# Kernel optimization log

Hardware: AMD Instinct MI355X
Metric: run time of the kernel (lower is better)

## Reference

```python
import jax, jax.numpy as jnp
import numpy as np

ALPHA = 0.2        # LeakyReLU slope inside attention layers
OUT_SLOPE = 0.01   # F.leaky_relu default slope on the final output
EPS = 1e-16        # guards isolated nodes (pyGAT divides by rowsum directly)


def _sp_layer(x, src, dst, W, a, concat, n_nodes):
    # x: [N, F_in], W: [F_in, F_out], a: [2*F_out]
    h = x @ W                                            # [N, F_out]
    eh = jnp.concatenate([h[src], h[dst]], axis=1)       # [E, 2*F_out]
    e = jnp.exp(-jax.nn.leaky_relu(eh @ a, ALPHA))       # [E] unnormalized attn
    denom = jax.ops.segment_sum(e, src, num_segments=n_nodes)          # [N]
    agg = jax.ops.segment_sum(e[:, None] * h[dst], src, num_segments=n_nodes)  # [N, F_out]
    hp = agg / (denom[:, None] + EPS)
    return jax.nn.elu(hp) if concat else hp


def _forward_one(xb, eib, W_heads, a_heads, W_out, a_out):
    n = xb.shape[0]
    src, dst = eib[0], eib[1]
    # independent heads (static small loop), concat on feature dim
    heads = [_sp_layer(xb, src, dst, W_heads[h], a_heads[h], True, n)
             for h in range(W_heads.shape[0])]
    xc = jnp.concatenate(heads, axis=1)                  # [N, nheads*nhid]
    out = _sp_layer(xc, src, dst, W_out, a_out, False, n)  # [N, nclass]
    return jax.nn.leaky_relu(out, OUT_SLOPE)


def setup_inputs() -> dict:
    key = jax.random.key(0)
    B, N, E = 8, 10000, 160000
    nfeat, nhid, nclass, nheads = 256, 64, 64, 8
    ks = jax.random.split(key, 6)
    x = jax.random.normal(ks[0], (B, N, nfeat), dtype=jnp.float32)
    edge_index = jax.random.randint(ks[1], (B, 2, E), 0, N, dtype=jnp.int32)
    # xavier-normal-ish init scales
    W_heads = jax.random.normal(ks[2], (nheads, nfeat, nhid), dtype=jnp.float32) * np.sqrt(2.0 / (nfeat + nhid))
    a_heads = jax.random.normal(ks[3], (nheads, 2 * nhid), dtype=jnp.float32) * np.sqrt(2.0 / (2 * nhid + 1))
    W_out = jax.random.normal(ks[4], (nheads * nhid, nclass), dtype=jnp.float32) * np.sqrt(2.0 / (nheads * nhid + nclass))
    a_out = jax.random.normal(ks[5], (2 * nclass,), dtype=jnp.float32) * np.sqrt(2.0 / (2 * nclass + 1))
    return {"x": x, "edge_index": edge_index, "W_heads": W_heads,
            "a_heads": a_heads, "W_out": W_out, "a_out": a_out, "batch_size": B}


def reference(x, edge_index, W_heads, a_heads, W_out, a_out, batch_size):
    # batch loop in the original is a pure map over graphs -> vmap
    return jax.vmap(lambda xb, eib: _forward_one(xb, eib, W_heads, a_heads, W_out, a_out))(x, edge_index)
```

## Files before the change

kernel.cpp:

```cpp
#include <hip/hip_runtime.h>
#include <cstdint>
#include <cstddef>

#define NND   10000
#define NED   160000
#define NB    8
#define NF    256
#define NHID  64
#define HEADS 8
#define F1    512
#define NCLS  64

#define NSH   8
#define NBUCK 40
#define CHUNK 4096

#define ALPHA_SLOPE 0.2f
#define OUT_SLOPE   0.01f
#define EPS         1e-16f

typedef unsigned short u16;
typedef short short8 __attribute__((ext_vector_type(8)));
typedef float f32x4 __attribute__((ext_vector_type(4)));

static const size_t B_WCHI = 0;
static const size_t B_WCLO = 262144;
static const size_t B_WOHI = 524288;
static const size_t B_WOLO = 589824;
static const size_t B_AS1  = 655360;
static const size_t B_AD1  = 3215360;
static const size_t B_AS2  = 5775360;
static const size_t B_AD2  = 6095360;
static const size_t B_CNT  = 6415360;
static const size_t B_BCUR = 6735360;
static const size_t B_ROWS = 6739456;
static const size_t B_TMP  = 7059520;
static const size_t B_DST  = 12179520;
static const size_t B_SCR  = 14739520;
#define ZSTRU 16000000ull
static const size_t S_PERZ = 2 * ZSTRU;

__device__ __forceinline__ u16 f32_to_bf16_rn(float f) {
  uint32_t u = __float_as_uint(f);
  uint32_t r = u + 0x7fffu + ((u >> 16) & 1u);
  return (u16)(r >> 16);
}
__device__ __forceinline__ float bf16_to_f32(u16 s) {
  return __uint_as_float((uint32_t)s << 16);
}
__device__ __forceinline__ void split1(float v, u16& h, u16& l) {
  h = f32_to_bf16_rn(v);
  float r = v - bf16_to_f32(h);
  l = f32_to_bf16_rn(r);
}

__global__ __launch_bounds__(256) void k_wsplit1(const float* __restrict__ Whd,
                                                 u16* __restrict__ hi,
                                                 u16* __restrict__ lo) {
  int idx = blockIdx.x * 256 + threadIdx.x;
  int n = idx >> 8, k = idx & 255;
  float v = Whd[(n >> 6) * (NF * NHID) + k * NHID + (n & 63)];
  u16 h, l; split1(v, h, l);
  hi[idx] = h; lo[idx] = l;
}
__global__ __launch_bounds__(256) void k_wsplit2(const float* __restrict__ Wo,
                                                 u16* __restrict__ hi,
                                                 u16* __restrict__ lo) {
  int idx = blockIdx.x * 256 + threadIdx.x;
  int n = idx >> 9, k = idx & 511;
  float v = Wo[k * NCLS + n];
  u16 h, l; split1(v, h, l);
  hi[idx] = h; lo[idx] = l;
}

__global__ __launch_bounds__(256) void k_gemm1(
    const float* __restrict__ x,
    const u16* __restrict__ Bhi, const u16* __restrict__ Blo,
    u16* __restrict__ h1_s,
    const float* __restrict__ avec,
    float* __restrict__ as_g, float* __restrict__ ad_g,
    int base_b, int zsh) {
  __shared__ u16 As_hi[64][40];
  __shared__ u16 As_lo[64][40];
  __shared__ u16 Bs_hi[256][40];
  __shared__ u16 Bs_lo[256][40];

  const int zmask = (1 << zsh) - 1;
  const int z = blockIdx.x & zmask;
  const int wg = blockIdx.x >> zsh;
  const int b = base_b + z;
  const float* A = x + (size_t)b * NND * NF;
  u16* C = h1_s + (size_t)z * ZSTRU;
  float* as_ = as_g + (size_t)b * NND * 8;
  float* ad_ = ad_g + (size_t)b * NND * 8;

  const int m0 = (wg >> 1) * 64;
  const int by = wg & 1;

  const int tid = threadIdx.x;
  const int lane = tid & 63;
  const int w = tid >> 6;
  const int lm = lane & 15;
  const int lkg = lane >> 4;
  const int hb = by * 4 + w;

  f32x4 acc[4][4];
#pragma unroll
  for (int mi = 0; mi < 4; ++mi)
#pragma unroll
    for (int nj = 0; nj < 4; ++nj) acc[mi][nj] = 0.f;

  for (int kk = 0; kk < NF; kk += 32) {
    __syncthreads();
#pragma unroll
    for (int u = 0; u < 2; ++u) {
      int e = u * 256 + tid;
      int rr = e >> 3, kf = (e & 7) * 4;
      int gm = m0 + rr;
      float4 v = make_float4(0.f, 0.f, 0.f, 0.f);
      if (gm < NND) v = *(const float4*)(A + (size_t)gm * NF + kk + kf);
      ushort4 hv, lv;
      split1(v.x, hv.x, lv.x); split1(v.y, hv.y, lv.y);
      split1(v.z, hv.z, lv.z); split1(v.w, hv.w, lv.w);
      *(ushort4*)&As_hi[rr][kf] = hv;
      *(ushort4*)&As_lo[rr][kf] = lv;
    }
#pragma unroll
    for (int u = 0; u < 8; ++u) {
      int e = u * 256 + tid;
      int n = e >> 3, kf = (e & 7) * 4;
      size_t g = (size_t)(by * 256 + n) * NF + kk + kf;
      *(ushort4*)&Bs_hi[n][kf] = *(const ushort4*)(Bhi + g);
      *(ushort4*)&Bs_lo[n][kf] = *(const ushort4*)(Blo + g);
    }
    __syncthreads();

    short8 ah[4], al[4], bh[4], bl[4];
#pragma unroll
    for (int mi = 0; mi < 4; ++mi) {
      int row = mi * 16 + lm;
      ah[mi] = *(const short8*)&As_hi[row][lkg * 8];
      al[mi] = *(const short8*)&As_lo[row][lkg * 8];
    }
#pragma unroll
    for (int nj = 0; nj < 4; ++nj) {
      int row = w * 64 + nj * 16 + lm;
      bh[nj] = *(const short8*)&Bs_hi[row][lkg * 8];
      bl[nj] = *(const short8*)&Bs_lo[row][lkg * 8];
    }
#pragma unroll
    for (int mi = 0; mi < 4; ++mi)
#pragma unroll
      for (int nj = 0; nj < 4; ++nj) {
        acc[mi][nj] = __builtin_amdgcn_mfma_f32_16x16x32_bf16(ah[mi], bh[nj], acc[mi][nj], 0, 0, 0);
        acc[mi][nj] = __builtin_amdgcn_mfma_f32_16x16x32_bf16(ah[mi], bl[nj], acc[mi][nj], 0, 0, 0);
        acc[mi][nj] = __builtin_amdgcn_mfma_f32_16x16x32_bf16(al[mi], bh[nj], acc[mi][nj], 0, 0, 0);
      }
  }

  float a_sv[4], a_dv[4];
#pragma unroll
  for (int nj = 0; nj < 4; ++nj) {
    a_sv[nj] = avec[hb * 128 + nj * 16 + lm];
    a_dv[nj] = avec[hb * 128 + 64 + nj * 16 + lm];
  }
  const int n0 = by * 256 + w * 64;
#pragma unroll
  for (int mi = 0; mi < 4; ++mi) {
#pragma unroll
    for (int rr = 0; rr < 4; ++rr) {
      int gm = m0 + mi * 16 + lkg * 4 + rr;
      float ps = acc[mi][0][rr] * a_sv[0] + acc[mi][1][rr] * a_sv[1] +
                 acc[mi][2][rr] * a_sv[2] + acc[mi][3][rr] * a_sv[3];
      float pd = acc[mi][0][rr] * a_dv[0] + acc[mi][1][rr] * a_dv[1] +
                 acc[mi][2][rr] * a_dv[2] + acc[mi][3][rr] * a_dv[3];
#pragma unroll
      for (int off = 1; off < 16; off <<= 1) {
        ps += __shfl_xor(ps, off, 16);
        pd += __shfl_xor(pd, off, 16);
      }
      if (gm < NND) {
#pragma unroll
        for (int nj = 0; nj < 4; ++nj)
          C[(size_t)gm * F1 + n0 + nj * 16 + lm] = f32_to_bf16_rn(acc[mi][nj][rr]);
        if (lm == 0) {
          as_[(size_t)gm * 8 + hb] = ps;
          ad_[(size_t)gm * 8 + hb] = pd;
        }
      }
    }
  }
}

__global__ __launch_bounds__(256) void k_gemm2(
    const u16* __restrict__ Ahi_s, const u16* __restrict__ Alo_s,
    const u16* __restrict__ Bhi, const u16* __restrict__ Blo,
    u16* __restrict__ C_s,
    const float* __restrict__ avec,
    float* __restrict__ as_g, float* __restrict__ ad_g,
    int base_b, int zsh) {
  __shared__ u16 As_hi[64][40];
  __shared__ u16 As_lo[64][40];
  __shared__ u16 Bs_hi[64][40];
  __shared__ u16 Bs_lo[64][40];

  const int zmask = (1 << zsh) - 1;
  const int z = blockIdx.x & zmask;
  const int wg = blockIdx.x >> zsh;
  const int b = base_b + z;
  const u16* Ahi = Ahi_s + (size_t)z * ZSTRU;
  const u16* Alo = Alo_s + (size_t)z * ZSTRU;
  u16* C = C_s + (size_t)z * ZSTRU;
  float* as_ = as_g + (size_t)b * NND;
  float* ad_ = ad_g + (size_t)b * NND;

  const int tid = threadIdx.x;
  const int lane = tid & 63;
  const int w = tid >> 6;
  const int lm = lane & 15;
  const int lkg = lane >> 4;
  const int m0 = wg * 64;

  f32x4 acc[4];
#pragma unroll
  for (int j = 0; j < 4; ++j) acc[j] = 0.f;

  for (int kk = 0; kk < F1; kk += 32) {
    __syncthreads();
#pragma unroll
    for (int u = 0; u < 2; ++u) {
      int e = u * 256 + tid;
      int rr = e >> 3, kf = (e & 7) * 4;
      int gm = m0 + rr;
      ushort4 hv = make_ushort4(0, 0, 0, 0), lv = make_ushort4(0, 0, 0, 0);
      if (gm < NND) {
        size_t g = (size_t)gm * F1 + kk + kf;
        hv = *(const ushort4*)(Ahi + g);
        lv = *(const ushort4*)(Alo + g);
      }
      *(ushort4*)&As_hi[rr][kf] = hv;
      *(ushort4*)&As_lo[rr][kf] = lv;
    }
#pragma unroll
    for (int u = 0; u < 2; ++u) {
      int e = u * 256 + tid;
      int n = e >> 3, kf = (e & 7) * 4;
      size_t g = (size_t)n * F1 + kk + kf;
      *(ushort4*)&Bs_hi[n][kf] = *(const ushort4*)(Bhi + g);
      *(ushort4*)&Bs_lo[n][kf] = *(const ushort4*)(Blo + g);
    }
    __syncthreads();

    short8 ah, al, bh[4], bl[4];
    {
      int row = w * 16 + lm;
      ah = *(const short8*)&As_hi[row][lkg * 8];
      al = *(const short8*)&As_lo[row][lkg * 8];
    }
#pragma unroll
    for (int nj = 0; nj < 4; ++nj) {
      int row = nj * 16 + lm;
      bh[nj] = *(const short8*)&Bs_hi[row][lkg * 8];
      bl[nj] = *(const short8*)&Bs_lo[row][lkg * 8];
    }
#pragma unroll
    for (int nj = 0; nj < 4; ++nj) {
      acc[nj] = __builtin_amdgcn_mfma_f32_16x16x32_bf16(ah, bh[nj], acc[nj], 0, 0, 0);
      acc[nj] = __builtin_amdgcn_mfma_f32_16x16x32_bf16(ah, bl[nj], acc[nj], 0, 0, 0);
      acc[nj] = __builtin_amdgcn_mfma_f32_16x16x32_bf16(al, bh[nj], acc[nj], 0, 0, 0);
    }
  }

  float a_sv[4], a_dv[4];
#pragma unroll
  for (int nj = 0; nj < 4; ++nj) {
    a_sv[nj] = avec[nj * 16 + lm];
    a_dv[nj] = avec[64 + nj * 16 + lm];
  }
#pragma unroll
  for (int rr = 0; rr < 4; ++rr) {
    int gm = m0 + w * 16 + lkg * 4 + rr;
    float ps = acc[0][rr] * a_sv[0] + acc[1][rr] * a_sv[1] +
               acc[2][rr] * a_sv[2] + acc[3][rr] * a_sv[3];
    float pd = acc[0][rr] * a_dv[0] + acc[1][rr] * a_dv[1] +
               acc[2][rr] * a_dv[2] + acc[3][rr] * a_dv[3];
#pragma unroll
    for (int off = 1; off < 16; off <<= 1) {
      ps += __shfl_xor(ps, off, 16);
      pd += __shfl_xor(pd, off, 16);
    }
    if (gm < NND) {
#pragma unroll
      for (int nj = 0; nj < 4; ++nj)
        C[(size_t)gm * NCLS + nj * 16 + lm] = f32_to_bf16_rn(acc[nj][rr]);
      if (lm == 0) {
        as_[gm] = ps;
        ad_[gm] = pd;
      }
    }
  }
}


__global__ __launch_bounds__(256) void k_hist(const int* __restrict__ ei,
                                              int* __restrict__ counts) {
  int b = blockIdx.y;
  int e4 = (blockIdx.x * 256 + threadIdx.x) * 4;
  if (e4 < NED) {
    int4 s = *(const int4*)(ei + (size_t)b * 2 * NED + e4);
    atomicAdd(&counts[b * NND + s.x], 1);
    atomicAdd(&counts[b * NND + s.y], 1);
    atomicAdd(&counts[b * NND + s.z], 1);
    atomicAdd(&counts[b * NND + s.w], 1);
  }
}

__global__ __launch_bounds__(1024) void k_scan(const int* __restrict__ counts,
                                               int* __restrict__ rows) {
  __shared__ int lds[1024];
  const int b = blockIdx.x;
  const int tid = threadIdx.x;
  const int* cb = counts + b * NND;
  int* rb = rows + b * (NND + 1);
  int v[10];
  int s = 0;
  int base = tid * 10;
#pragma unroll
  for (int j = 0; j < 10; ++j) {
    int i = base + j;
    v[j] = (i < NND) ? cb[i] : 0;
    s += v[j];
  }
  lds[tid] = s;
  __syncthreads();
  for (int off = 1; off < 1024; off <<= 1) {
    int t = (tid >= off) ? lds[tid - off] : 0;
    __syncthreads();
    lds[tid] += t;
    __syncthreads();
  }
  int run = lds[tid] - s;
#pragma unroll
  for (int j = 0; j < 10; ++j) {
    int i = base + j;
    if (i < NND) rb[i] = run;
    run += v[j];
  }
  if (tid == 1023) rb[NND] = run;
}

__global__ __launch_bounds__(256) void k_scat_a(const int* __restrict__ ei,
                                                const int* __restrict__ rows,
                                                int* __restrict__ bcur,
                                                unsigned* __restrict__ tmp) {
  __shared__ unsigned stage[CHUNK];
  __shared__ int cnt[NBUCK], off[NBUCK], cur[NBUCK], gb[NBUCK];
  const int b = blockIdx.y;
  const int e0 = blockIdx.x * CHUNK;
  const int nE = min(CHUNK, NED - e0);
  const int tid = threadIdx.x;
  const int* sb = ei + (size_t)b * 2 * NED;
  const int* db = sb + NED;

  for (int k = tid; k < NBUCK; k += 256) cnt[k] = 0;
  __syncthreads();
  for (int j = tid; j < nE; j += 256)
    atomicAdd(&cnt[sb[e0 + j] >> NSH], 1);
  __syncthreads();
  if (tid == 0) {
    int run = 0;
    for (int k = 0; k < NBUCK; ++k) { off[k] = run; run += cnt[k]; }
  }
  __syncthreads();
  for (int k = tid; k < NBUCK; k += 256) cur[k] = off[k];
  __syncthreads();
  for (int j = tid; j < nE; j += 256) {
    int s = sb[e0 + j], d = db[e0 + j];
    int p = atomicAdd(&cur[s >> NSH], 1);
    stage[p] = ((unsigned)s << 16) | (unsigned)d;
  }
  __syncthreads();
  for (int k = tid; k < NBUCK; k += 256) {
    int c = cnt[k];
    gb[k] = c ? rows[b * (NND + 1) + (k << NSH)] + atomicAdd(&bcur[b * NBUCK + k], c)
              : 0;
  }
  __syncthreads();
  for (int i = tid; i < nE; i += 256) {
    unsigned p = stage[i];
    int k = (int)(p >> 16) >> NSH;
    tmp[(size_t)b * NED + gb[k] + (i - off[k])] = p;
  }
}

__global__ __launch_bounds__(256) void k_scat_b(const int* __restrict__ rows,
                                                const unsigned* __restrict__ tmp,
                                                u16* __restrict__ dst_s) {
  __shared__ int cur[256];
  const int k = blockIdx.x, b = blockIdx.y;
  const int* rb = rows + b * (NND + 1);
  const int n0 = k << NSH;
  const int tid = threadIdx.x;
  cur[tid] = rb[min(n0 + tid, NND)];
  __syncthreads();
  const int beg = rb[n0];
  const int end = rb[min(n0 + 256, NND)];
  for (int i = beg + tid; i < end; i += 256) {
    unsigned p = tmp[(size_t)b * NED + i];
    int pos = atomicAdd(&cur[(int)(p >> 16) - n0], 1);
    dst_s[(size_t)b * NED + pos] = (u16)(p & 0xffffu);
  }
}

#define UPK8(q, e) do { \
  acc[0] = fmaf(e, __uint_as_float((q).x << 16), acc[0]); \
  acc[1] = fmaf(e, __uint_as_float((q).x & 0xffff0000u), acc[1]); \
  acc[2] = fmaf(e, __uint_as_float((q).y << 16), acc[2]); \
  acc[3] = fmaf(e, __uint_as_float((q).y & 0xffff0000u), acc[3]); \
  acc[4] = fmaf(e, __uint_as_float((q).z << 16), acc[4]); \
  acc[5] = fmaf(e, __uint_as_float((q).z & 0xffff0000u), acc[5]); \
  acc[6] = fmaf(e, __uint_as_float((q).w << 16), acc[6]); \
  acc[7] = fmaf(e, __uint_as_float((q).w & 0xffff0000u), acc[7]); \
} while (0)

#define LKY(t) ((t) >= 0.f ? (t) : ALPHA_SLOPE * (t))

__global__ __launch_bounds__(256) void k_agg1(
    const int* __restrict__ rows_g, const u16* __restrict__ dst_g,
    const u16* __restrict__ h1_s,
    const float* __restrict__ as_g, const float* __restrict__ ad_g,
    u16* __restrict__ xchi_s, u16* __restrict__ xclo_s,
    int base_b, int zsh) {
  const int zmask = (1 << zsh) - 1;
  const int z = blockIdx.x & zmask;
  const int idx = blockIdx.x >> zsh;
  const int b = base_b + z;
  const int* rows = rows_g + (size_t)b * (NND + 1);
  const u16* dst = dst_g + (size_t)b * NED;
  const u16* h1 = h1_s + (size_t)z * ZSTRU;
  const float* as_ = as_g + (size_t)b * NND * 8;
  const float* ad_ = ad_g + (size_t)b * NND * 8;
  u16* xh = xchi_s + (size_t)z * ZSTRU;
  u16* xl = xclo_s + (size_t)z * ZSTRU;

  int lane = threadIdx.x & 63;
  int n = (idx * 256 + threadIdx.x) >> 6;
  if (n >= NND) return;
  const int hh = lane >> 3;
  const float asv = as_[n * 8 + hh];
  int beg = rows[n], end = rows[n + 1];
  float acc[8] = {};
  float den = 0.f;
  int i = beg;
  for (; i + 4 <= end; i += 4) {
    int d0 = dst[i], d1 = dst[i + 1], d2 = dst[i + 2], d3 = dst[i + 3];
    float t0 = LKY(asv + ad_[d0 * 8 + hh]);
    float t1 = LKY(asv + ad_[d1 * 8 + hh]);
    float t2 = LKY(asv + ad_[d2 * 8 + hh]);
    float t3 = LKY(asv + ad_[d3 * 8 + hh]);
    float e0 = __expf(-t0), e1 = __expf(-t1);
    float e2 = __expf(-t2), e3 = __expf(-t3);
    uint4 q0 = *((const uint4*)(h1 + (size_t)d0 * F1) + lane);
    uint4 q1 = *((const uint4*)(h1 + (size_t)d1 * F1) + lane);
    uint4 q2 = *((const uint4*)(h1 + (size_t)d2 * F1) + lane);
    uint4 q3 = *((const uint4*)(h1 + (size_t)d3 * F1) + lane);
    UPK8(q0, e0); UPK8(q1, e1); UPK8(q2, e2); UPK8(q3, e3);
    den += (e0 + e1) + (e2 + e3);
  }
  for (; i < end; ++i) {
    int d0 = dst[i];
    float t0 = LKY(asv + ad_[d0 * 8 + hh]);
    float e0 = __expf(-t0);
    uint4 q0 = *((const uint4*)(h1 + (size_t)d0 * F1) + lane);
    UPK8(q0, e0);
    den += e0;
  }
  float inv = 1.f / (den + EPS);
  u16 oh[8], ol[8];
#pragma unroll
  for (int j = 0; j < 8; ++j) {
    float v = acc[j] * inv;
    v = v > 0.f ? v : expm1f(v);
    split1(v, oh[j], ol[j]);
  }
  size_t wo = (size_t)n * F1 + lane * 8;
  *(ushort4*)(xh + wo) = make_ushort4(oh[0], oh[1], oh[2], oh[3]);
  *(ushort4*)(xh + wo + 4) = make_ushort4(oh[4], oh[5], oh[6], oh[7]);
  *(ushort4*)(xl + wo) = make_ushort4(ol[0], ol[1], ol[2], ol[3]);
  *(ushort4*)(xl + wo + 4) = make_ushort4(ol[4], ol[5], ol[6], ol[7]);
}

__global__ __launch_bounds__(256) void k_agg2(
    const int* __restrict__ rows_g, const u16* __restrict__ dst_g,
    const u16* __restrict__ h2_s,
    const float* __restrict__ as_g, const float* __restrict__ ad_g,
    float* __restrict__ out, int base_b, int zsh) {
  const int zmask = (1 << zsh) - 1;
  const int z = blockIdx.x & zmask;
  const int idx = blockIdx.x >> zsh;
  const int b = base_b + z;
  const int* rows = rows_g + (size_t)b * (NND + 1);
  const u16* dst = dst_g + (size_t)b * NED;
  const u16* h2 = h2_s + (size_t)z * ZSTRU;
  const float* as_ = as_g + (size_t)b * NND;
  const float* ad_ = ad_g + (size_t)b * NND;
  float* ob = out + (size_t)b * NND * NCLS;

  int lane = threadIdx.x & 63;
  int n = (idx * 256 + threadIdx.x) >> 6;
  if (n >= NND) return;
  const float asv = as_[n];
  int beg = rows[n], end = rows[n + 1];
  float acc = 0.f, den = 0.f;
  int i = beg;
  for (; i + 4 <= end; i += 4) {
    int d0 = dst[i], d1 = dst[i + 1], d2 = dst[i + 2], d3 = dst[i + 3];
    float t0 = LKY(asv + ad_[d0]);
    float t1 = LKY(asv + ad_[d1]);
    float t2 = LKY(asv + ad_[d2]);
    float t3 = LKY(asv + ad_[d3]);
    float e0 = __expf(-t0), e1 = __expf(-t1);
    float e2 = __expf(-t2), e3 = __expf(-t3);
    float h0 = bf16_to_f32(h2[(size_t)d0 * NCLS + lane]);
    float h1v = bf16_to_f32(h2[(size_t)d1 * NCLS + lane]);
    float h2v = bf16_to_f32(h2[(size_t)d2 * NCLS + lane]);
    float h3v = bf16_to_f32(h2[(size_t)d3 * NCLS + lane]);
    acc = fmaf(e0, h0, acc); acc = fmaf(e1, h1v, acc);
    acc = fmaf(e2, h2v, acc); acc = fmaf(e3, h3v, acc);
    den += (e0 + e1) + (e2 + e3);
  }
  for (; i < end; ++i) {
    int d0 = dst[i];
    float t0 = LKY(asv + ad_[d0]);
    float e0 = __expf(-t0);
    acc = fmaf(e0, bf16_to_f32(h2[(size_t)d0 * NCLS + lane]), acc);
    den += e0;
  }
  float v = acc / (den + EPS);
  ob[(size_t)n * NCLS + lane] = v >= 0.f ? v : OUT_SLOPE * v;
}

extern "C" void kernel_launch(void* const* d_in, const int* in_sizes, int n_in,
                              void* d_out, int out_size, void* d_ws, size_t ws_size,
                              hipStream_t stream) {
  const float* x       = (const float*)d_in[0];
  const int*   ei      = (const int*)d_in[1];
  const float* W_heads = (const float*)d_in[2];
  const float* a_heads = (const float*)d_in[3];
  const float* W_out   = (const float*)d_in[4];
  const float* a_out   = (const float*)d_in[5];
  float* out = (float*)d_out;

  char* base = (char*)d_ws;
  u16* wchi = (u16*)(base + B_WCHI);
  u16* wclo = (u16*)(base + B_WCLO);
  u16* wohi = (u16*)(base + B_WOHI);
  u16* wolo = (u16*)(base + B_WOLO);
  float* as1 = (float*)(base + B_AS1);
  float* ad1 = (float*)(base + B_AD1);
  float* as2 = (float*)(base + B_AS2);
  float* ad2 = (float*)(base + B_AD2);
  int* counts    = (int*)(base + B_CNT);
  int* bcur      = (int*)(base + B_BCUR);
  int* rows      = (int*)(base + B_ROWS);
  unsigned* tmp  = (unsigned*)(base + B_TMP);
  u16* dst_s     = (u16*)(base + B_DST);
  u16* scr       = (u16*)(base + B_SCR);

  int Z = 1, zsh = 0;
  if (ws_size >= B_SCR + 8 * S_PERZ) { Z = 8; zsh = 3; }
  else if (ws_size >= B_SCR + 4 * S_PERZ) { Z = 4; zsh = 2; }
  else if (ws_size >= B_SCR + 2 * S_PERZ) { Z = 2; zsh = 1; }

  u16* xchi = scr + 0;
  u16* xclo = scr + 5120000;
  u16* h1   = scr + 10240000;
  u16* h2   = scr + 15360000;

  k_wsplit1<<<(F1 * NF) / 256, 256, 0, stream>>>(W_heads, wchi, wclo);
  k_wsplit2<<<(NCLS * F1) / 256, 256, 0, stream>>>(W_out, wohi, wolo);

  hipMemsetAsync(counts, 0, B_ROWS - B_CNT, stream);
  k_hist<<<dim3((NED / 4 + 255) / 256, NB), 256, 0, stream>>>(ei, counts);
  k_scan<<<NB, 1024, 0, stream>>>(counts, rows);
  k_scat_a<<<dim3((NED + CHUNK - 1) / CHUNK, NB), 256, 0, stream>>>(ei, rows, bcur, tmp);
  k_scat_b<<<dim3(NBUCK, NB), 256, 0, stream>>>(rows, tmp, dst_s);

  const int nwg1 = ((NND + 63) / 64) * 2;
  const int nwg2 = (NND + 63) / 64;
  for (int bb = 0; bb < NB; bb += Z) {
    k_gemm1<<<dim3(nwg1 << zsh), 256, 0, stream>>>(
        x, wchi, wclo, h1, a_heads, as1, ad1, bb, zsh);
    k_agg1<<<dim3(2500 << zsh), 256, 0, stream>>>(rows, dst_s, h1, as1, ad1,
                                                  xchi, xclo, bb, zsh);
    k_gemm2<<<dim3(nwg2 << zsh), 256, 0, stream>>>(
        xchi, xclo, wohi, wolo, h2, a_out, as2, ad2, bb, zsh);
    k_agg2<<<dim3(2500 << zsh), 256, 0, stream>>>(rows, dst_s, h2, as2, ad2,
                                                  out, bb, zsh);
  }
  (void)in_sizes; (void)n_in; (void)out_size;
}
```

Baseline: 475.8 us.

## Prepack W in MFMA fragment order and make h1 head-major for per-head aggregation

```diff
diff --git a/kernel.cpp b/kernel.cpp
--- a/kernel.cpp
+++ b/kernel.cpp
@@ -57,11 +57,27 @@
 __global__ __launch_bounds__(256) void k_wsplit1(const float* __restrict__ Whd,
                                                  u16* __restrict__ hi,
                                                  u16* __restrict__ lo) {
-  int idx = blockIdx.x * 256 + threadIdx.x;
-  int n = idx >> 8, k = idx & 255;
-  float v = Whd[(n >> 6) * (NF * NHID) + k * NHID + (n & 63)];
-  u16 h, l; split1(v, h, l);
-  hi[idx] = h; lo[idx] = l;
+  int t = blockIdx.x * 256 + threadIdx.x;
+  int lane = t & 63;
+  int frag = t >> 6;
+  int nj = frag & 3;
+  int w  = (frag >> 2) & 3;
+  int ts = (frag >> 4) & 7;
+  int by = frag >> 7;
+  int lm = lane & 15, lkg = lane >> 4;
+  int n = by * 256 + w * 64 + nj * 16 + lm;
+  int h = n >> 6, nc = n & 63;
+  u16 hv[8], lv[8];
+#pragma unroll
+  for (int j = 0; j < 8; ++j) {
+    int k = ts * 32 + lkg * 8 + j;
+    split1(Whd[h * (NF * NHID) + k * NHID + nc], hv[j], lv[j]);
+  }
+  size_t o = (size_t)t * 8;
+  *(ushort4*)(hi + o) = make_ushort4(hv[0], hv[1], hv[2], hv[3]);
+  *(ushort4*)(hi + o + 4) = make_ushort4(hv[4], hv[5], hv[6], hv[7]);
+  *(ushort4*)(lo + o) = make_ushort4(lv[0], lv[1], lv[2], lv[3]);
+  *(ushort4*)(lo + o + 4) = make_ushort4(lv[4], lv[5], lv[6], lv[7]);
 }
 __global__ __launch_bounds__(256) void k_wsplit2(const float* __restrict__ Wo,
                                                  u16* __restrict__ hi,
@@ -75,15 +91,13 @@
 
 __global__ __launch_bounds__(256) void k_gemm1(
     const float* __restrict__ x,
-    const u16* __restrict__ Bhi, const u16* __restrict__ Blo,
+    const u16* __restrict__ Bfh, const u16* __restrict__ Bfl,
     u16* __restrict__ h1_s,
     const float* __restrict__ avec,
     float* __restrict__ as_g, float* __restrict__ ad_g,
     int base_b, int zsh) {
   __shared__ u16 As_hi[64][40];
   __shared__ u16 As_lo[64][40];
-  __shared__ u16 Bs_hi[256][40];
-  __shared__ u16 Bs_lo[256][40];
 
   const int zmask = (1 << zsh) - 1;
   const int z = blockIdx.x & zmask;
@@ -110,7 +124,8 @@
 #pragma unroll
     for (int nj = 0; nj < 4; ++nj) acc[mi][nj] = 0.f;
 
-  for (int kk = 0; kk < NF; kk += 32) {
+  for (int t = 0; t < 8; ++t) {
+    const int kk = t * 32;
     __syncthreads();
 #pragma unroll
     for (int u = 0; u < 2; ++u) {
@@ -125,28 +140,23 @@
       *(ushort4*)&As_hi[rr][kf] = hv;
       *(ushort4*)&As_lo[rr][kf] = lv;
     }
-#pragma unroll
-    for (int u = 0; u < 8; ++u) {
-      int e = u * 256 + tid;
-      int n = e >> 3, kf = (e & 7) * 4;
-      size_t g = (size_t)(by * 256 + n) * NF + kk + kf;
-      *(ushort4*)&Bs_hi[n][kf] = *(const ushort4*)(Bhi + g);
-      *(ushort4*)&Bs_lo[n][kf] = *(const ushort4*)(Blo + g);
+    short8 bh[4], bl[4];
+    {
+      size_t fb = (((size_t)(by * 8 + t) * 4 + w) * 4) * 512 + (size_t)lane * 8;
+#pragma unroll
+      for (int nj = 0; nj < 4; ++nj) {
+        bh[nj] = *(const short8*)(Bfh + fb + nj * 512);
+        bl[nj] = *(const short8*)(Bfl + fb + nj * 512);
+      }
     }
     __syncthreads();
 
-    short8 ah[4], al[4], bh[4], bl[4];
+    short8 ah[4], al[4];
 #pragma unroll
     for (int mi = 0; mi < 4; ++mi) {
       int row = mi * 16 + lm;
       ah[mi] = *(const short8*)&As_hi[row][lkg * 8];
       al[mi] = *(const short8*)&As_lo[row][lkg * 8];
-    }
-#pragma unroll
-    for (int nj = 0; nj < 4; ++nj) {
-      int row = w * 64 + nj * 16 + lm;
-      bh[nj] = *(const short8*)&Bs_hi[row][lkg * 8];
-      bl[nj] = *(const short8*)&Bs_lo[row][lkg * 8];
     }
 #pragma unroll
     for (int mi = 0; mi < 4; ++mi)
@@ -164,7 +174,6 @@
     a_sv[nj] = avec[hb * 128 + nj * 16 + lm];
     a_dv[nj] = avec[hb * 128 + 64 + nj * 16 + lm];
   }
-  const int n0 = by * 256 + w * 64;
 #pragma unroll
   for (int mi = 0; mi < 4; ++mi) {
 #pragma unroll
@@ -182,7 +191,7 @@
       if (gm < NND) {
 #pragma unroll
         for (int nj = 0; nj < 4; ++nj)
-          C[(size_t)gm * F1 + n0 + nj * 16 + lm] = f32_to_bf16_rn(acc[mi][nj][rr]);
+          C[((size_t)hb * NND + gm) * 64 + nj * 16 + lm] = f32_to_bf16_rn(acc[mi][nj][rr]);
         if (lm == 0) {
           as_[(size_t)gm * 8 + hb] = ps;
           ad_[(size_t)gm * 8 + hb] = pd;
@@ -412,17 +421,6 @@
   }
 }
 
-#define UPK8(q, e) do { \
-  acc[0] = fmaf(e, __uint_as_float((q).x << 16), acc[0]); \
-  acc[1] = fmaf(e, __uint_as_float((q).x & 0xffff0000u), acc[1]); \
-  acc[2] = fmaf(e, __uint_as_float((q).y << 16), acc[2]); \
-  acc[3] = fmaf(e, __uint_as_float((q).y & 0xffff0000u), acc[3]); \
-  acc[4] = fmaf(e, __uint_as_float((q).z << 16), acc[4]); \
-  acc[5] = fmaf(e, __uint_as_float((q).z & 0xffff0000u), acc[5]); \
-  acc[6] = fmaf(e, __uint_as_float((q).w << 16), acc[6]); \
-  acc[7] = fmaf(e, __uint_as_float((q).w & 0xffff0000u), acc[7]); \
-} while (0)
-
 #define LKY(t) ((t) >= 0.f ? (t) : ALPHA_SLOPE * (t))
 
 __global__ __launch_bounds__(256) void k_agg1(
@@ -434,60 +432,52 @@
   const int zmask = (1 << zsh) - 1;
   const int z = blockIdx.x & zmask;
   const int idx = blockIdx.x >> zsh;
+  const int h = idx / 2500;
+  const int nb = idx - h * 2500;
   const int b = base_b + z;
   const int* rows = rows_g + (size_t)b * (NND + 1);
   const u16* dst = dst_g + (size_t)b * NED;
-  const u16* h1 = h1_s + (size_t)z * ZSTRU;
+  const u16* h1 = h1_s + (size_t)z * ZSTRU + (size_t)h * NND * 64;
   const float* as_ = as_g + (size_t)b * NND * 8;
   const float* ad_ = ad_g + (size_t)b * NND * 8;
   u16* xh = xchi_s + (size_t)z * ZSTRU;
   u16* xl = xclo_s + (size_t)z * ZSTRU;
 
-  int lane = threadIdx.x & 63;
-  int n = (idx * 256 + threadIdx.x) >> 6;
-  if (n >= NND) return;
-  const int hh = lane >> 3;
-  const float asv = as_[n * 8 + hh];
+  const int lane = threadIdx.x & 63;
+  const int n = nb * 4 + (threadIdx.x >> 6);
+  const float asv = as_[n * 8 + h];
   int beg = rows[n], end = rows[n + 1];
-  float acc[8] = {};
-  float den = 0.f;
+  float acc = 0.f, den = 0.f;
   int i = beg;
   for (; i + 4 <= end; i += 4) {
     int d0 = dst[i], d1 = dst[i + 1], d2 = dst[i + 2], d3 = dst[i + 3];
-    float t0 = LKY(asv + ad_[d0 * 8 + hh]);
-    float t1 = LKY(asv + ad_[d1 * 8 + hh]);
-    float t2 = LKY(asv + ad_[d2 * 8 + hh]);
-    float t3 = LKY(asv + ad_[d3 * 8 + hh]);
+    float t0 = LKY(asv + ad_[d0 * 8 + h]);
+    float t1 = LKY(asv + ad_[d1 * 8 + h]);
+    float t2 = LKY(asv + ad_[d2 * 8 + h]);
+    float t3 = LKY(asv + ad_[d3 * 8 + h]);
     float e0 = __expf(-t0), e1 = __expf(-t1);
     float e2 = __expf(-t2), e3 = __expf(-t3);
-    uint4 q0 = *((const uint4*)(h1 + (size_t)d0 * F1) + lane);
-    uint4 q1 = *((const uint4*)(h1 + (size_t)d1 * F1) + lane);
-    uint4 q2 = *((const uint4*)(h1 + (size_t)d2 * F1) + lane);
-    uint4 q3 = *((const uint4*)(h1 + (size_t)d3 * F1) + lane);
-    UPK8(q0, e0); UPK8(q1, e1); UPK8(q2, e2); UPK8(q3, e3);
+    float h0 = bf16_to_f32(h1[(size_t)d0 * 64 + lane]);
+    float h1v = bf16_to_f32(h1[(size_t)d1 * 64 + lane]);
+    float h2v = bf16_to_f32(h1[(size_t)d2 * 64 + lane]);
+    float h3v = bf16_to_f32(h1[(size_t)d3 * 64 + lane]);
+    acc = fmaf(e0, h0, acc); acc = fmaf(e1, h1v, acc);
+    acc = fmaf(e2, h2v, acc); acc = fmaf(e3, h3v, acc);
     den += (e0 + e1) + (e2 + e3);
   }
   for (; i < end; ++i) {
     int d0 = dst[i];
-    float t0 = LKY(asv + ad_[d0 * 8 + hh]);
+    float t0 = LKY(asv + ad_[d0 * 8 + h]);
     float e0 = __expf(-t0);
-    uint4 q0 = *((const uint4*)(h1 + (size_t)d0 * F1) + lane);
-    UPK8(q0, e0);
+    acc = fmaf(e0, bf16_to_f32(h1[(size_t)d0 * 64 + lane]), acc);
     den += e0;
   }
-  float inv = 1.f / (den + EPS);
-  u16 oh[8], ol[8];
-#pragma unroll
-  for (int j = 0; j < 8; ++j) {
-    float v = acc[j] * inv;
-    v = v > 0.f ? v : expm1f(v);
-    split1(v, oh[j], ol[j]);
-  }
-  size_t wo = (size_t)n * F1 + lane * 8;
-  *(ushort4*)(xh + wo) = make_ushort4(oh[0], oh[1], oh[2], oh[3]);
-  *(ushort4*)(xh + wo + 4) = make_ushort4(oh[4], oh[5], oh[6], oh[7]);
-  *(ushort4*)(xl + wo) = make_ushort4(ol[0], ol[1], ol[2], ol[3]);
-  *(ushort4*)(xl + wo + 4) = make_ushort4(ol[4], ol[5], ol[6], ol[7]);
+  float v = acc / (den + EPS);
+  v = v > 0.f ? v : expm1f(v);
+  u16 hh, ll; split1(v, hh, ll);
+  size_t wo = (size_t)n * F1 + h * 64 + lane;
+  xh[wo] = hh;
+  xl[wo] = ll;
 }
 
 __global__ __launch_bounds__(256) void k_agg2(
@@ -577,7 +567,7 @@
   u16* h1   = scr + 10240000;
   u16* h2   = scr + 15360000;
 
-  k_wsplit1<<<(F1 * NF) / 256, 256, 0, stream>>>(W_heads, wchi, wclo);
+  k_wsplit1<<<64, 256, 0, stream>>>(W_heads, wchi, wclo);
   k_wsplit2<<<(NCLS * F1) / 256, 256, 0, stream>>>(W_out, wohi, wolo);
 
   hipMemsetAsync(counts, 0, B_ROWS - B_CNT, stream);
@@ -591,8 +581,8 @@
   for (int bb = 0; bb < NB; bb += Z) {
     k_gemm1<<<dim3(nwg1 << zsh), 256, 0, stream>>>(
         x, wchi, wclo, h1, a_heads, as1, ad1, bb, zsh);
-    k_agg1<<<dim3(2500 << zsh), 256, 0, stream>>>(rows, dst_s, h1, as1, ad1,
-                                                  xchi, xclo, bb, zsh);
+    k_agg1<<<dim3((HEADS * 2500) << zsh), 256, 0, stream>>>(
+        rows, dst_s, h1, as1, ad1, xchi, xclo, bb, zsh);
     k_gemm2<<<dim3(nwg2 << zsh), 256, 0, stream>>>(
         xchi, xclo, wohi, wolo, h2, a_out, as2, ad2, bb, zsh);
     k_agg2<<<dim3(2500 << zsh), 256, 0, stream>>>(rows, dst_s, h2, as2, ad2,
```

After: 665.2 us. 39.8% more time.

## Pre-pack GEMM1 weights in MFMA fragment order and load B directly to registers

Applied to the files above, without the earlier changes.

```diff
diff --git a/kernel.cpp b/kernel.cpp
--- a/kernel.cpp
+++ b/kernel.cpp
@@ -57,11 +57,27 @@
 __global__ __launch_bounds__(256) void k_wsplit1(const float* __restrict__ Whd,
                                                  u16* __restrict__ hi,
                                                  u16* __restrict__ lo) {
-  int idx = blockIdx.x * 256 + threadIdx.x;
-  int n = idx >> 8, k = idx & 255;
-  float v = Whd[(n >> 6) * (NF * NHID) + k * NHID + (n & 63)];
-  u16 h, l; split1(v, h, l);
-  hi[idx] = h; lo[idx] = l;
+  int t = blockIdx.x * 256 + threadIdx.x;
+  int lane = t & 63;
+  int frag = t >> 6;
+  int nj = frag & 3;
+  int w  = (frag >> 2) & 3;
+  int ts = (frag >> 4) & 7;
+  int by = frag >> 7;
+  int lm = lane & 15, lkg = lane >> 4;
+  int n = by * 256 + w * 64 + nj * 16 + lm;
+  int h = n >> 6, nc = n & 63;
+  u16 hv[8], lv[8];
+#pragma unroll
+  for (int j = 0; j < 8; ++j) {
+    int k = ts * 32 + lkg * 8 + j;
+    split1(Whd[h * (NF * NHID) + k * NHID + nc], hv[j], lv[j]);
+  }
+  size_t o = (size_t)t * 8;
+  *(ushort4*)(hi + o) = make_ushort4(hv[0], hv[1], hv[2], hv[3]);
+  *(ushort4*)(hi + o + 4) = make_ushort4(hv[4], hv[5], hv[6], hv[7]);
+  *(ushort4*)(lo + o) = make_ushort4(lv[0], lv[1], lv[2], lv[3]);
+  *(ushort4*)(lo + o + 4) = make_ushort4(lv[4], lv[5], lv[6], lv[7]);
 }
 __global__ __launch_bounds__(256) void k_wsplit2(const float* __restrict__ Wo,
                                                  u16* __restrict__ hi,
@@ -75,15 +91,13 @@
 
 __global__ __launch_bounds__(256) void k_gemm1(
     const float* __restrict__ x,
-    const u16* __restrict__ Bhi, const u16* __restrict__ Blo,
+    const u16* __restrict__ Bfh, const u16* __restrict__ Bfl,
     u16* __restrict__ h1_s,
     const float* __restrict__ avec,
     float* __restrict__ as_g, float* __restrict__ ad_g,
     int base_b, int zsh) {
   __shared__ u16 As_hi[64][40];
   __shared__ u16 As_lo[64][40];
-  __shared__ u16 Bs_hi[256][40];
-  __shared__ u16 Bs_lo[256][40];
 
   const int zmask = (1 << zsh) - 1;
   const int z = blockIdx.x & zmask;
@@ -110,7 +124,8 @@
 #pragma unroll
     for (int nj = 0; nj < 4; ++nj) acc[mi][nj] = 0.f;
 
-  for (int kk = 0; kk < NF; kk += 32) {
+  for (int t = 0; t < 8; ++t) {
+    const int kk = t * 32;
     __syncthreads();
 #pragma unroll
     for (int u = 0; u < 2; ++u) {
@@ -125,28 +140,23 @@
       *(ushort4*)&As_hi[rr][kf] = hv;
       *(ushort4*)&As_lo[rr][kf] = lv;
     }
-#pragma unroll
-    for (int u = 0; u < 8; ++u) {
-      int e = u * 256 + tid;
-      int n = e >> 3, kf = (e & 7) * 4;
-      size_t g = (size_t)(by * 256 + n) * NF + kk + kf;
-      *(ushort4*)&Bs_hi[n][kf] = *(const ushort4*)(Bhi + g);
-      *(ushort4*)&Bs_lo[n][kf] = *(const ushort4*)(Blo + g);
+    short8 bh[4], bl[4];
+    {
+      size_t fb = (((size_t)(by * 8 + t) * 4 + w) * 4) * 512 + (size_t)lane * 8;
+#pragma unroll
+      for (int nj = 0; nj < 4; ++nj) {
+        bh[nj] = *(const short8*)(Bfh + fb + nj * 512);
+        bl[nj] = *(const short8*)(Bfl + fb + nj * 512);
+      }
     }
     __syncthreads();
 
-    short8 ah[4], al[4], bh[4], bl[4];
+    short8 ah[4], al[4];
 #pragma unroll
     for (int mi = 0; mi < 4; ++mi) {
       int row = mi * 16 + lm;
       ah[mi] = *(const short8*)&As_hi[row][lkg * 8];
       al[mi] = *(const short8*)&As_lo[row][lkg * 8];
-    }
-#pragma unroll
-    for (int nj = 0; nj < 4; ++nj) {
-      int row = w * 64 + nj * 16 + lm;
-      bh[nj] = *(const short8*)&Bs_hi[row][lkg * 8];
-      bl[nj] = *(const short8*)&Bs_lo[row][lkg * 8];
     }
 #pragma unroll
     for (int mi = 0; mi < 4; ++mi)
@@ -577,7 +587,7 @@
   u16* h1   = scr + 10240000;
   u16* h2   = scr + 15360000;
 
-  k_wsplit1<<<(F1 * NF) / 256, 256, 0, stream>>>(W_heads, wchi, wclo);
+  k_wsplit1<<<64, 256, 0, stream>>>(W_heads, wchi, wclo);
   k_wsplit2<<<(NCLS * F1) / 256, 256, 0, stream>>>(W_out, wohi, wolo);
 
   hipMemsetAsync(counts, 0, B_ROWS - B_CNT, stream);
```

Result: faster. 454.0 us (-4.6%).
